# Optimization experiments

Measured on AMD Instinct MI355X. Metric: run time of the kernel, lower is better.

The kernel has to match this reference:

```python
import jax, jax.numpy as jnp
import numpy as np

TAU = 0.07
K = 50
EPS = 1e-8


def _flat_norm(x):
    # [B, C, H, W] -> [B*H*W, C], L2-normalized along C
    B, C = x.shape[0], x.shape[1]
    x = jnp.moveaxis(x, 1, -1).reshape(-1, C)
    n = jnp.linalg.norm(x, axis=-1, keepdims=True)
    return x / jnp.maximum(n, 1e-12)


def setup_inputs() -> dict:
    key = jax.random.key(0)
    ks = jax.random.split(key, 5)
    shp = (2, 128, 64, 64)
    lshp = (2, 4, 64, 64)
    return {
        "input": jax.random.normal(ks[0], shp, dtype=jnp.float32),
        "positive": jax.random.normal(ks[1], shp, dtype=jnp.float32),
        "negative": jax.random.normal(ks[2], shp, dtype=jnp.float32),
        "input_logits": jax.random.normal(ks[3], lshp, dtype=jnp.float32),
        "negative_logits": jax.random.normal(ks[4], lshp, dtype=jnp.float32),
    }


def reference(input, positive, negative, input_logits, negative_logits):
    norm_input = _flat_norm(input)        # [N, C]
    norm_positive = _flat_norm(positive)  # [N, C]
    norm_negative = _flat_norm(negative)  # [N, C]

    # check_input: multi-class logits branch (softmax over class dim, then max)
    in_probs = jax.nn.softmax(input_logits, axis=1)
    neg_probs = jax.nn.softmax(negative_logits, axis=1)
    seg_input = jnp.argmax(in_probs, axis=1).reshape(-1)       # [N] int
    seg_negative = jnp.argmax(neg_probs, axis=1).reshape(-1)   # [N] int
    negative_prob = jnp.max(neg_probs, axis=1).reshape(-1)     # [N] float

    # positive cosine similarity (unit vectors -> dot product)
    pos_sim = jnp.sum(norm_input * norm_positive, axis=-1)     # [N]

    # mask[i, j] = (seg_input[j] != seg_negative[i]) * negative_prob[i]
    diff = (seg_input[None, :] != seg_negative[:, None]).astype(jnp.float16)
    masked = diff.astype(jnp.float32) * negative_prob[:, None]  # [N, N]

    # top-k over dim=0 (negatives) for each input column j -> indices [N, K]
    _, idx = jax.lax.top_k(masked.T, K)                         # [N, K]
    sampled = norm_negative[idx]                                # [N, K, C]

    neg_sim = jnp.einsum('nkc,nc->nk', sampled, norm_input)     # [N, K]
    nominator = jnp.exp(pos_sim / TAU)                          # [N]
    denominator = jnp.sum(jnp.exp(neg_sim / TAU), axis=1) + nominator
    loss = -jnp.mean(jnp.log(nominator / (denominator + EPS)))

    alter_sim = jnp.einsum('nkc,nc->nk', sampled, norm_positive)
    alter_den = jnp.sum(jnp.exp(alter_sim / TAU), axis=1) + nominator
    alter_loss = -jnp.mean(jnp.log(nominator / (alter_den + EPS)))

    return loss + alter_loss
```

## Files before the change

### kernel.cpp

```cpp
#include <hip/hip_runtime.h>
#include <math.h>

#define TAU_INV (1.0f / 0.07f)
#define KSEL 50
#define KPAD 64
#define NPIX 8192
#define CCH 128
#define HWSZ 4096
#define NCLS 4
#define EPSL 1e-8f
#define NBINS 1026
#define PXT 16
#define SROW 132

__global__ void init_kernel(float* __restrict__ acc, int* __restrict__ cnt) {
    if (threadIdx.x == 0) acc[0] = 0.0f;
    if (threadIdx.x < NCLS) cnt[threadIdx.x] = 0;
}

__global__ void __launch_bounds__(256) mega_kernel(
        const float* __restrict__ input, const float* __restrict__ positive,
        const float* __restrict__ negative,
        const float* __restrict__ ilog, const float* __restrict__ nlog,
        float* __restrict__ ni, float* __restrict__ np_, float* __restrict__ nn,
        int* __restrict__ seg_neg, float* __restrict__ neg_prob,
        int* __restrict__ gcnt, int* __restrict__ perm) {
    __shared__ float tile[CCH][65];
    __shared__ float partial[4][64];
    __shared__ float invn[64];
    __shared__ int lcnt[NCLS], lbase[NCLS];

    int t = threadIdx.x;
    int blk = blockIdx.x;

    if (blk < 384) {
        int tensor = blk >> 7, chunk = blk & 127;
        const float* src = (tensor == 0) ? input : (tensor == 1) ? positive : negative;
        float*       dst = (tensor == 0) ? ni    : (tensor == 1) ? np_      : nn;

        int n0 = chunk * 64;
        int b = n0 >> 12, hw0 = n0 & (HWSZ - 1);
        const float* base = src + (size_t)b * CCH * HWSZ + hw0;

        #pragma unroll
        for (int i = 0; i < 32; ++i) {
            int lin = t + i * 256;
            int c = lin >> 6, hw = lin & 63;
            tile[c][hw] = base[(size_t)c * HWSZ + hw];
        }
        __syncthreads();

        int nof = t & 63, part = t >> 6;
        float s = 0.f;
        #pragma unroll
        for (int j = 0; j < 32; ++j) {
            float v = tile[part * 32 + j][nof];
            s += v * v;
        }
        partial[part][nof] = s;
        __syncthreads();
        if (t < 64) {
            float tot = partial[0][t] + partial[1][t] + partial[2][t] + partial[3][t];
            invn[t] = 1.0f / fmaxf(sqrtf(tot), 1e-12f);
        }
        __syncthreads();

        #pragma unroll
        for (int i = 0; i < 32; ++i) {
            int lin = t + i * 256;
            int nf = lin >> 7, c = lin & 127;
            dst[(size_t)(n0 + nf) * CCH + c] = tile[c][nf] * invn[nf];
        }
    } else {
        if (t < NCLS) lcnt[t] = 0;
        __syncthreads();

        int n = (blk - 384) * 256 + t;
        int b = n >> 12, hw = n & (HWSZ - 1);

        const float* pi = ilog + (size_t)b * NCLS * HWSZ + hw;
        float l0 = pi[0], l1 = pi[HWSZ], l2 = pi[2 * HWSZ], l3 = pi[3 * HWSZ];
        int bi = 0; float bv = l0;
        if (l1 > bv) { bv = l1; bi = 1; }
        if (l2 > bv) { bv = l2; bi = 2; }
        if (l3 > bv) { bv = l3; bi = 3; }

        const float* pn = nlog + (size_t)b * NCLS * HWSZ + hw;
        float m0 = pn[0], m1 = pn[HWSZ], m2 = pn[2 * HWSZ], m3 = pn[3 * HWSZ];
        int ci = 0; float cv = m0;
        if (m1 > cv) { cv = m1; ci = 1; }
        if (m2 > cv) { cv = m2; ci = 2; }
        if (m3 > cv) { cv = m3; ci = 3; }
        seg_neg[n] = ci;
        float s = expf(m0 - cv) + expf(m1 - cv) + expf(m2 - cv) + expf(m3 - cv);
        neg_prob[n] = 1.0f / s;

        int lpos = atomicAdd(&lcnt[bi], 1);
        __syncthreads();
        if (t < NCLS) lbase[t] = atomicAdd(&gcnt[t], lcnt[t]);
        __syncthreads();
        perm[bi * NPIX + lbase[bi] + lpos] = n;
    }
}

__global__ void __launch_bounds__(1024) topk_kernel(const int* __restrict__ seg_neg,
                                                    const float* __restrict__ neg_prob,
                                                    int* __restrict__ topk) {
    __shared__ unsigned hist[NBINS];
    __shared__ unsigned long long cand[2048];
    __shared__ unsigned above_cnt, cand_cnt;
    __shared__ int sB, sc0;

    int c = blockIdx.x, t = threadIdx.x;

    for (int i = t; i < NBINS; i += 1024) hist[i] = 0;
    if (t == 0) { above_cnt = 0; cand_cnt = 0; }
    __syncthreads();

    unsigned keys[8]; int bins[8];
    #pragma unroll
    for (int s = 0; s < 8; ++s) {
        int i = t + s * 1024;
        float v = (seg_neg[i] != c) ? neg_prob[i] : 0.0f;
        unsigned key = __float_as_uint(v);
        int bin = (key < 0x3E800000u) ? 0 : (int)(1u + ((key - 0x3E800000u) >> 14));
        keys[s] = key; bins[s] = bin;
        atomicAdd(&hist[bin], 1u);
    }
    __syncthreads();

    if (t == 0) {
        unsigned cum = 0; int B = 0;
        for (int b = NBINS - 1; b >= 0; --b) {
            unsigned h = hist[b];
            if (cum + h >= KSEL) { B = b; break; }
            cum += h;
        }
        sB = B; sc0 = (int)cum;
    }
    __syncthreads();
    int B = sB, c0 = sc0;

    #pragma unroll
    for (int s = 0; s < 8; ++s) {
        int i = t + s * 1024;
        if (bins[s] > B) {
            unsigned pos = atomicAdd(&above_cnt, 1u);
            topk[c * KSEL + pos] = i;
        } else if (bins[s] == B) {
            unsigned j = atomicAdd(&cand_cnt, 1u);
            if (j < 2048)
                cand[j] = ((unsigned long long)keys[s] << 32) |
                          (unsigned long long)(0xFFFFFFFFu - (unsigned)i);
        }
    }
    __syncthreads();

    int m = KSEL - c0;
    int cb = (int)cand_cnt; if (cb > 2048) cb = 2048;
    if (t < 64) {
        for (int r = 0; r < m; ++r) {
            unsigned long long best = 0;
            for (int j = t; j < cb; j += 64) {
                unsigned long long v = cand[j];
                if (v > best) best = v;
            }
            #pragma unroll
            for (int off = 32; off; off >>= 1) {
                unsigned long long o = __shfl_xor(best, off);
                if (o > best) best = o;
            }
            if (t == 0) topk[c * KSEL + c0 + r] = (int)(0xFFFFFFFFu - (unsigned)(best & 0xFFFFFFFFull));
            for (int j = t; j < cb; j += 64)
                if (cand[j] == best) cand[j] = 0;
        }
    }
}

__global__ void __launch_bounds__(256) loss_kernel(
        const float* __restrict__ ni, const float* __restrict__ npos,
        const float* __restrict__ nn, const int* __restrict__ topk,
        const int* __restrict__ perm, const int* __restrict__ cnt,
        float* __restrict__ acc) {
    __shared__ float Sl[KPAD * SROW];
    __shared__ float Xl[PXT * SROW];
    __shared__ float Pl[PXT * SROW];
    __shared__ float bsum[4];

    int c = blockIdx.y;
    int count = cnt[c];
    int start = blockIdx.x * PXT;
    if (start >= count) return;
    int t = threadIdx.x;

    {
        int row = t >> 2;
        int ch0 = (t & 3) * 32;
        float* dst = &Sl[row * SROW + ch0];
        if (row < KSEL) {
            const float* src = nn + (size_t)topk[c * KSEL + row] * CCH + ch0;
            #pragma unroll
            for (int i = 0; i < 8; ++i)
                ((float4*)dst)[i] = ((const float4*)src)[i];
        } else {
            float4 z = make_float4(0.f, 0.f, 0.f, 0.f);
            #pragma unroll
            for (int i = 0; i < 8; ++i)
                ((float4*)dst)[i] = z;
        }
    }
    {
        int row = t >> 4;
        int slot = start + row;
        int px = perm[c * NPIX + ((slot < count) ? slot : start)];
        int ch0 = (t & 15) * 8;
        const float* sx = ni + (size_t)px * CCH + ch0;
        const float* sp = npos + (size_t)px * CCH + ch0;
        float* dx = &Xl[row * SROW + ch0];
        float* dp = &Pl[row * SROW + ch0];
        ((float4*)dx)[0] = ((const float4*)sx)[0];
        ((float4*)dx)[1] = ((const float4*)sx)[1];
        ((float4*)dp)[0] = ((const float4*)sp)[0];
        ((float4*)dp)[1] = ((const float4*)sp)[1];
    }
    __syncthreads();

    int ktid = t & 15, pxid = t >> 4;
    float acc_i[4] = {0.f, 0.f, 0.f, 0.f};
    float acc_p[4] = {0.f, 0.f, 0.f, 0.f};
    float ps = 0.f;
    const float* Xr = &Xl[pxid * SROW];
    const float* Pr = &Pl[pxid * SROW];

    #pragma unroll 4
    for (int ch = 0; ch < CCH; ch += 4) {
        float4 xv = *(const float4*)&Xr[ch];
        float4 pv = *(const float4*)&Pr[ch];
        ps += xv.x * pv.x + xv.y * pv.y + xv.z * pv.z + xv.w * pv.w;
        #pragma unroll
        for (int r = 0; r < 4; ++r) {
            float4 sv = *(const float4*)&Sl[(ktid + r * 16) * SROW + ch];
            acc_i[r] += sv.x * xv.x + sv.y * xv.y + sv.z * xv.z + sv.w * xv.w;
            acc_p[r] += sv.x * pv.x + sv.y * pv.y + sv.z * pv.z + sv.w * pv.w;
        }
    }

    float si = 0.f, spp = 0.f;
    #pragma unroll
    for (int r = 0; r < 4; ++r) {
        si  += expf(acc_i[r] * TAU_INV);
        spp += expf(acc_p[r] * TAU_INV);
    }
    #pragma unroll
    for (int off = 1; off < 16; off <<= 1) {
        si  += __shfl_xor(si, off);
        spp += __shfl_xor(spp, off);
    }

    float v = 0.f;
    if (ktid == 0 && (start + pxid) < count) {
        si  -= (float)(KPAD - KSEL);
        spp -= (float)(KPAD - KSEL);
        float nom = expf(ps * TAU_INV);
        float li = -logf(nom / (si + nom + EPSL));
        float lp = -logf(nom / (spp + nom + EPSL));
        v = li + lp;
    }
    v += __shfl_xor(v, 16);
    v += __shfl_xor(v, 32);
    int w = t >> 6;
    if ((t & 63) == 0) bsum[w] = v;
    __syncthreads();
    if (t == 0) atomicAdd(acc, bsum[0] + bsum[1] + bsum[2] + bsum[3]);
}

__global__ void fin_kernel(const float* __restrict__ acc, float* __restrict__ out) {
    out[0] = acc[0] * (1.0f / (float)NPIX);
}

extern "C" void kernel_launch(void* const* d_in, const int* in_sizes, int n_in,
                              void* d_out, int out_size, void* d_ws, size_t ws_size,
                              hipStream_t stream) {
    const float* input      = (const float*)d_in[0];
    const float* positive   = (const float*)d_in[1];
    const float* negative   = (const float*)d_in[2];
    const float* in_logits  = (const float*)d_in[3];
    const float* neg_logits = (const float*)d_in[4];
    float* out = (float*)d_out;

    float* ws  = (float*)d_ws;
    float* ni  = ws;
    float* np_ = ws + 1048576;
    float* nn  = ws + 2097152;
    int*   seg_neg  = (int*)(ws + 3145728);
    float* neg_prob = (float*)(seg_neg + NPIX);
    int*   topk     = (int*)(neg_prob + NPIX);
    int*   cnt      = topk + 256;
    float* acc      = (float*)(cnt + 64);
    int*   perm     = (int*)(acc + 64);

    init_kernel<<<1, 64, 0, stream>>>(acc, cnt);
    mega_kernel<<<416, 256, 0, stream>>>(input, positive, negative,
                                         in_logits, neg_logits,
                                         ni, np_, nn, seg_neg, neg_prob, cnt, perm);
    topk_kernel<<<NCLS, 1024, 0, stream>>>(seg_neg, neg_prob, topk);
    dim3 lgrid(NPIX / PXT, NCLS);
    loss_kernel<<<lgrid, 256, 0, stream>>>(ni, np_, nn, topk, perm, cnt, acc);
    fin_kernel<<<1, 1, 0, stream>>>(acc, out);
}
```

Baseline: 104.0 us.

## Fold init and finalize kernels into neighbors, move pixel bucketing into topk

Removes the init and fin kernel launches. The zeroing of the output moves into topk_kernel and the 1/N scaling moves into the per-pixel loss. Per-class pixel bucketing (perm and cnt) moves from mega_kernel's global atomics into topk_kernel, where each class block scans seg_in with a shared counter. A two-level coarse histogram scan replaces the serial 1026-bin threshold search. This trims launch overhead and serial work, at the cost of extra seg_in traffic and a slightly longer topk kernel.

```diff
diff --git a/kernel.cpp b/kernel.cpp
--- a/kernel.cpp
+++ b/kernel.cpp
@@ -13,22 +13,16 @@
 #define PXT 16
 #define SROW 132
 
-__global__ void init_kernel(float* __restrict__ acc, int* __restrict__ cnt) {
-    if (threadIdx.x == 0) acc[0] = 0.0f;
-    if (threadIdx.x < NCLS) cnt[threadIdx.x] = 0;
-}
-
 __global__ void __launch_bounds__(256) mega_kernel(
         const float* __restrict__ input, const float* __restrict__ positive,
         const float* __restrict__ negative,
         const float* __restrict__ ilog, const float* __restrict__ nlog,
         float* __restrict__ ni, float* __restrict__ np_, float* __restrict__ nn,
-        int* __restrict__ seg_neg, float* __restrict__ neg_prob,
-        int* __restrict__ gcnt, int* __restrict__ perm) {
+        int* __restrict__ seg_in, int* __restrict__ seg_neg,
+        float* __restrict__ neg_prob) {
     __shared__ float tile[CCH][65];
     __shared__ float partial[4][64];
     __shared__ float invn[64];
-    __shared__ int lcnt[NCLS], lbase[NCLS];
 
     int t = threadIdx.x;
     int blk = blockIdx.x;
@@ -72,9 +66,6 @@
             dst[(size_t)(n0 + nf) * CCH + c] = tile[c][nf] * invn[nf];
         }
     } else {
-        if (t < NCLS) lcnt[t] = 0;
-        __syncthreads();
-
         int n = (blk - 384) * 256 + t;
         int b = n >> 12, hw = n & (HWSZ - 1);
 
@@ -84,6 +75,7 @@
         if (l1 > bv) { bv = l1; bi = 1; }
         if (l2 > bv) { bv = l2; bi = 2; }
         if (l3 > bv) { bv = l3; bi = 3; }
+        seg_in[n] = bi;
 
         const float* pn = nlog + (size_t)b * NCLS * HWSZ + hw;
         float m0 = pn[0], m1 = pn[HWSZ], m2 = pn[2 * HWSZ], m3 = pn[3 * HWSZ];
@@ -94,27 +86,26 @@
         seg_neg[n] = ci;
         float s = expf(m0 - cv) + expf(m1 - cv) + expf(m2 - cv) + expf(m3 - cv);
         neg_prob[n] = 1.0f / s;
-
-        int lpos = atomicAdd(&lcnt[bi], 1);
-        __syncthreads();
-        if (t < NCLS) lbase[t] = atomicAdd(&gcnt[t], lcnt[t]);
-        __syncthreads();
-        perm[bi * NPIX + lbase[bi] + lpos] = n;
     }
 }
 
-__global__ void __launch_bounds__(1024) topk_kernel(const int* __restrict__ seg_neg,
-                                                    const float* __restrict__ neg_prob,
-                                                    int* __restrict__ topk) {
+__global__ void __launch_bounds__(1024) topk_kernel(
+        const int* __restrict__ seg_in, const int* __restrict__ seg_neg,
+        const float* __restrict__ neg_prob,
+        int* __restrict__ topk, int* __restrict__ perm, int* __restrict__ cnt,
+        float* __restrict__ out) {
     __shared__ unsigned hist[NBINS];
+    __shared__ unsigned coarse[33];
     __shared__ unsigned long long cand[2048];
-    __shared__ unsigned above_cnt, cand_cnt;
+    __shared__ unsigned above_cnt, cand_cnt, bucket_cnt;
     __shared__ int sB, sc0;
 
     int c = blockIdx.x, t = threadIdx.x;
+    if (c == 0 && t == 0) out[0] = 0.0f;
 
     for (int i = t; i < NBINS; i += 1024) hist[i] = 0;
-    if (t == 0) { above_cnt = 0; cand_cnt = 0; }
+    if (t < 33) coarse[t] = 0;
+    if (t == 0) { above_cnt = 0; cand_cnt = 0; bucket_cnt = 0; }
     __syncthreads();
 
     unsigned keys[8]; int bins[8];
@@ -126,12 +117,27 @@
         int bin = (key < 0x3E800000u) ? 0 : (int)(1u + ((key - 0x3E800000u) >> 14));
         keys[s] = key; bins[s] = bin;
         atomicAdd(&hist[bin], 1u);
-    }
+        if (seg_in[i] == c) {
+            unsigned p = atomicAdd(&bucket_cnt, 1u);
+            perm[c * NPIX + p] = i;
+        }
+    }
+    __syncthreads();
+    if (t == 0) cnt[c] = (int)bucket_cnt;
+
+    for (int i = t; i < NBINS; i += 1024) atomicAdd(&coarse[i >> 5], hist[i]);
     __syncthreads();
 
     if (t == 0) {
-        unsigned cum = 0; int B = 0;
-        for (int b = NBINS - 1; b >= 0; --b) {
+        unsigned cum = 0; int j = 32;
+        for (; j > 0; --j) {
+            unsigned h = coarse[j];
+            if (cum + h >= KSEL) break;
+            cum += h;
+        }
+        int hi = j * 32 + 31; if (hi > NBINS - 1) hi = NBINS - 1;
+        int B = 0;
+        for (int b = hi; b >= j * 32; --b) {
             unsigned h = hist[b];
             if (cum + h >= KSEL) { B = b; break; }
             cum += h;
@@ -181,7 +187,7 @@
         const float* __restrict__ ni, const float* __restrict__ npos,
         const float* __restrict__ nn, const int* __restrict__ topk,
         const int* __restrict__ perm, const int* __restrict__ cnt,
-        float* __restrict__ acc) {
+        float* __restrict__ out) {
     __shared__ float Sl[KPAD * SROW];
     __shared__ float Xl[PXT * SROW];
     __shared__ float Pl[PXT * SROW];
@@ -264,18 +270,14 @@
         float nom = expf(ps * TAU_INV);
         float li = -logf(nom / (si + nom + EPSL));
         float lp = -logf(nom / (spp + nom + EPSL));
-        v = li + lp;
+        v = (li + lp) * (1.0f / (float)NPIX);
     }
     v += __shfl_xor(v, 16);
     v += __shfl_xor(v, 32);
     int w = t >> 6;
     if ((t & 63) == 0) bsum[w] = v;
     __syncthreads();
-    if (t == 0) atomicAdd(acc, bsum[0] + bsum[1] + bsum[2] + bsum[3]);
-}
-
-__global__ void fin_kernel(const float* __restrict__ acc, float* __restrict__ out) {
-    out[0] = acc[0] * (1.0f / (float)NPIX);
+    if (t == 0) atomicAdd(out, bsum[0] + bsum[1] + bsum[2] + bsum[3]);
 }
 
 extern "C" void kernel_launch(void* const* d_in, const int* in_sizes, int n_in,
@@ -292,19 +294,18 @@
     float* ni  = ws;
     float* np_ = ws + 1048576;
     float* nn  = ws + 2097152;
-    int*   seg_neg  = (int*)(ws + 3145728);
+    int*   seg_in   = (int*)(ws + 3145728);
+    int*   seg_neg  = seg_in + NPIX;
     float* neg_prob = (float*)(seg_neg + NPIX);
     int*   topk     = (int*)(neg_prob + NPIX);
     int*   cnt      = topk + 256;
-    float* acc      = (float*)(cnt + 64);
-    int*   perm     = (int*)(acc + 64);
-
-    init_kernel<<<1, 64, 0, stream>>>(acc, cnt);
+    int*   perm     = cnt + 64;
+
     mega_kernel<<<416, 256, 0, stream>>>(input, positive, negative,
                                          in_logits, neg_logits,
-                                         ni, np_, nn, seg_neg, neg_prob, cnt, perm);
-    topk_kernel<<<NCLS, 1024, 0, stream>>>(seg_neg, neg_prob, topk);
+                                         ni, np_, nn, seg_in, seg_neg, neg_prob);
+    topk_kernel<<<NCLS, 1024, 0, stream>>>(seg_in, seg_neg, neg_prob,
+                                           topk, perm, cnt, out);
     dim3 lgrid(NPIX / PXT, NCLS);
-    loss_kernel<<<lgrid, 256, 0, stream>>>(ni, np_, nn, topk, perm, cnt, acc);
-    fin_kernel<<<1, 1, 0, stream>>>(acc, out);
+    loss_kernel<<<lgrid, 256, 0, stream>>>(ni, np_, nn, topk, perm, cnt, out);
 }
```

Measured after the change: 101.8 us. 1.02x faster.
